# Kernel tuning notes

Measured on AMD Instinct MI355X. Metric: run time of the kernel, lower is better.

## Reference

```python
import jax, jax.numpy as jnp
import numpy as np

# module constants (from init_kwargs)
CS, NV, ED = 8, 4, 32          # codebook_size, num_variables, embedding_dim
VIEWS, D, KSZ = 3, 16, 3        # num_input_channels, depth, kernel_size
HW = 14                         # 7 * scale (scale=2)
CSP = 8                         # spatial of conv_shape after three valid 3x3 convs: 14->12->10->8
KSTATES = CS ** NV              # 4096 combinatorial discrete states


def _elu(x):
    return jnp.where(x > 0, x, jnp.expm1(x))


def _conv_t(x, w, b):
    # PyTorch ConvTranspose2d(stride=1, padding=0); w: (Cin, Cout, k, k)
    wf = jnp.flip(w, (2, 3)).transpose(1, 0, 2, 3)  # -> (Cout, Cin, k, k)
    p = w.shape[2] - 1
    y = jax.lax.conv_general_dilated(x, wf, (1, 1), [(p, p), (p, p)],
                                     dimension_numbers=('NCHW', 'OIHW', 'NCHW'))
    return y + b[None, :, None, None]


def setup_inputs() -> dict:
    key = jax.random.key(0)
    ks = jax.random.split(key, 10)
    rn = lambda k, shape, s=1.0: jax.random.normal(k, shape, jnp.float32) * s
    return {
        'x': rn(ks[0], (64, VIEWS, HW, HW)),
        'latent_embedding': rn(ks[1], (NV, CS, ED)),
        'lin_w': rn(ks[2], (VIEWS, ED * NV, 4 * D * CSP * CSP), 0.05),
        'lin_b': rn(ks[3], (VIEWS, 4 * D * CSP * CSP), 0.05),
        'w1': rn(ks[4], (VIEWS, 4 * D, 2 * D, KSZ, KSZ), 0.05),
        'b1': rn(ks[5], (VIEWS, 2 * D), 0.05),
        'w2': rn(ks[6], (VIEWS, 2 * D, D, KSZ, KSZ), 0.05),
        'b2': rn(ks[7], (VIEWS, D), 0.05),
        'w3': rn(ks[8], (VIEWS, D, 1, KSZ, KSZ), 0.05),
        'b3': rn(ks[9], (VIEWS, 1), 0.05),
    }


def reference(x, latent_embedding, lin_w, lin_b, w1, b1, w2, b2, w3, b3):
    # all combinations of codebook indices (itertools.product order): [K, NV]
    all_idcs = jnp.stack(
        jnp.meshgrid(*([jnp.arange(CS)] * NV), indexing='ij'), -1).reshape(-1, NV)
    # gather: z[k, v, :] = latent_embedding[v, all_idcs[k, v], :]
    z = latent_embedding[jnp.arange(NV)[None, :], all_idcs]       # [K, NV, ED]
    zf = z.reshape(KSTATES, NV * ED)                              # 'b n d -> b (n d)'

    def decode(lw, lb, W1, B1, W2, B2, W3, B3):
        h = (zf @ lw + lb).reshape(KSTATES, 4 * D, CSP, CSP)
        h = _elu(_conv_t(h, W1, B1))
        h = _elu(_conv_t(h, W2, B2))
        h = _conv_t(h, W3, B3)
        return h[:, 0]                                            # [K, HW, HW]

    m = jax.vmap(decode)(lin_w, lin_b, w1, b1, w2, b2, w3, b3)    # [views, K, HW, HW]
    m = jnp.transpose(m, (1, 0, 2, 3))                            # [K, views, HW, HW]

    # obs_logits = -0.5 * sum_{h,w} (m[None] - x[:, None])**2, computed without
    # materializing the [B, K, views, HW, HW] broadcast tensor
    m2 = jnp.sum(m * m, axis=(-2, -1))                            # [K, views]
    x2 = jnp.sum(x * x, axis=(-2, -1))                            # [B, views]
    cross = jnp.einsum('kvhw,bvhw->bkv', m, x)                    # [B, K, views]
    return -0.5 * (m2[None] + x2[:, None] - 2.0 * cross)          # [B, K, views]
```

## Files before the change

### kernel.cpp

```cpp
#include <hip/hip_runtime.h>
#include <cstddef>


typedef __attribute__((ext_vector_type(4))) float f32x4;
typedef _Float16 half8v __attribute__((ext_vector_type(8)));
typedef _Float16 half4v __attribute__((ext_vector_type(4)));
typedef _Float16 half2v __attribute__((ext_vector_type(2)));

static __device__ __forceinline__ float elu(float s) {
    float e = __expf(s) - 1.0f;
    return s > 0.f ? s : e;
}
static __device__ __forceinline__ float dot2acc(int hpair, int wpair, float acc) {
#if __has_builtin(__builtin_amdgcn_fdot2)
    return __builtin_amdgcn_fdot2(__builtin_bit_cast(half2v, hpair),
                                  __builtin_bit_cast(half2v, wpair), acc, false);
#else
    half2v h = __builtin_bit_cast(half2v, hpair);
    half2v w = __builtin_bit_cast(half2v, wpair);
    acc = fmaf((float)h.x, (float)w.x, acc);
    return fmaf((float)h.y, (float)w.y, acc);
#endif
}

__global__ __launch_bounds__(256) void pre_kernel(const float* __restrict__ x,
                                                  float* __restrict__ x2,
                                                  short* __restrict__ xB,
                                                  const float* __restrict__ w2,
                                                  short* __restrict__ Wf) {
    int v = blockIdx.x;
    int part = blockIdx.y;
    int t = threadIdx.x;
    if (part < 4) {
        int nb = part;
        short* xBv = xB + v * 14336 + nb * 3584;
        for (int idx = t; idx < 3584; idx += 256) {
            int j = idx & 7, lane = (idx >> 3) & 63, s = idx >> 9;
            int px = s * 32 + ((lane >> 4) << 3) + j;
            int b  = nb * 16 + (lane & 15);
            float val = (px < 196) ? x[(b * 3 + v) * 196 + px] : 0.f;
            _Float16 h = (_Float16)val;
            xBv[idx] = __builtin_bit_cast(short, h);
        }
    } else if (part == 4) {
        int w = t >> 6, lane = t & 63;
        for (int b = w; b < 64; b += 4) {
            const float* xp = x + (b * 3 + v) * 196;
            float s = 0.f;
            for (int px = lane; px < 196; px += 64) s = fmaf(xp[px], xp[px], s);
#pragma unroll
            for (int off = 32; off; off >>= 1) s += __shfl_down(s, off, 64);
            if (lane == 0) x2[v * 64 + b] = s;
        }
    } else if (t < 64) {
        int lane = t;
        const float* w2v = w2 + v * 32 * 16 * 9;
        int co = lane & 15;
        int cibase = (lane >> 4) * 8;
#pragma unroll
        for (int tap = 0; tap < 9; ++tap)
#pragma unroll
            for (int j = 0; j < 8; ++j) {
                _Float16 h = (_Float16)w2v[((cibase + j) * 16 + co) * 9 + tap];
                Wf[(((v * 9 + tap) * 64 + lane) << 3) + j] = __builtin_bit_cast(short, h);
            }
    }
}

__global__ __launch_bounds__(256) void pmat_kernel(const float* __restrict__ le,
                                                   const float* __restrict__ lin_w,
                                                   float* __restrict__ P3) {
    int o  = blockIdx.x * 256 + threadIdx.x;
    int vc = blockIdx.y;
    int v  = blockIdx.z;
    int vp = vc >> 3;
    const float* lwv = lin_w + (size_t)v * 128 * 4096;
    const float* lep = le + vc * 32;
    float acc = 0.f;
#pragma unroll
    for (int e = 0; e < 32; ++e)
        acc = fmaf(lep[e], lwv[(vp * 32 + e) * 4096 + o], acc);
    P3[((size_t)v * 32 + vc) * 4096 + o] = acc;
}

__global__ __launch_bounds__(320) void fold1_kernel(const float* __restrict__ P3,
                                                    const float* __restrict__ lin_b,
                                                    const float* __restrict__ w1,
                                                    const float* __restrict__ b1,
                                                    float* __restrict__ Qa,
                                                    float* __restrict__ Qb) {
    __shared__ float sPt[64 * 144];
    __shared__ float sW[16 * 32 * 9];
    int row = blockIdx.x;
    int v   = blockIdx.y;
    int z   = blockIdx.z;
    int t = threadIdx.x;
    const float* src = (row < 32) ? (P3 + ((size_t)v * 32 + row) * 4096)
                                  : (lin_b + v * 4096);
    float4* zp = (float4*)sPt;
    for (int i = t; i < 2304; i += 320) zp[i] = float4{0.f, 0.f, 0.f, 0.f};
    __syncthreads();
    for (int i = t; i < 4096; i += 320) {
        int ci = i >> 6, r = i & 63, y = r >> 3, xx = r & 7;
        sPt[ci * 144 + (xx + 2) * 12 + (y + 2)] = src[i];
    }
    const float* w1v = w1 + (size_t)v * 64 * 32 * 9;
    int co = t / 10, ox = t % 10;
    float acc[10];
#pragma unroll
    for (int i = 0; i < 10; ++i) acc[i] = 0.f;

    for (int c0 = z * 2; c0 < z * 2 + 2; ++c0) {
        __syncthreads();
        for (int i = t; i < 4608; i += 320) sW[i] = w1v[c0 * 4608 + i];
        __syncthreads();
#pragma unroll 2
        for (int ci = 0; ci < 16; ++ci) {
            const float* xp = sPt + (c0 * 16 + ci) * 144;
            const float* wp = sW + (ci * 32 + co) * 9;
            float wv[9];
#pragma unroll
            for (int j = 0; j < 9; ++j) wv[j] = wp[j];
#pragma unroll
            for (int b = 0; b < 3; ++b) {
                const float* colp = xp + (ox + 2 - b) * 12;
                float4 c0v = *(const float4*)(colp);
                float4 c1v = *(const float4*)(colp + 4);
                float4 c2v = *(const float4*)(colp + 8);
                float cv[12] = {c0v.x, c0v.y, c0v.z, c0v.w,
                                c1v.x, c1v.y, c1v.z, c1v.w,
                                c2v.x, c2v.y, c2v.z, c2v.w};
#pragma unroll
                for (int a = 0; a < 3; ++a) {
                    float wgt = wv[a * 3 + b];
#pragma unroll
                    for (int oy = 0; oy < 10; ++oy)
                        acc[oy] = fmaf(cv[oy + 2 - a], wgt, acc[oy]);
                }
            }
        }
    }
    float bb = (z == 0 && row == 32) ? b1[v * 32 + co] : 0.f;
    float* dst = (z == 0 ? Qa : Qb) + (size_t)v * 105600 + row * 3200;
#pragma unroll
    for (int oy = 0; oy < 10; ++oy)
        dst[(ox * 10 + oy) * 32 + co] = acc[oy] + bb;
}

__global__ __launch_bounds__(256) void pair_kernel(const float* __restrict__ Qa,
                                                   const float* __restrict__ Qb,
                                                   float* __restrict__ Q01,
                                                   float* __restrict__ Q23b) {
    int p = blockIdx.x;
    int half = blockIdx.y;
    int v = blockIdx.z;
    const float4* basea = (const float4*)(Qa + (size_t)v * 105600);
    const float4* baseb = (const float4*)(Qb + (size_t)v * 105600);
    if (half == 0) {
        const float4* ra = basea + (p >> 3) * 800;
        const float4* rb = baseb + (p >> 3) * 800;
        const float4* rc = basea + (8 + (p & 7)) * 800;
        const float4* rd = baseb + (8 + (p & 7)) * 800;
        float4* dst = (float4*)(Q01 + (size_t)v * 204800 + p * 3200);
        for (int i = threadIdx.x; i < 800; i += 256) {
            float4 a = ra[i], b = rb[i], c = rc[i], d = rd[i];
            dst[i] = float4{a.x + b.x + c.x + d.x, a.y + b.y + c.y + d.y,
                            a.z + b.z + c.z + d.z, a.w + b.w + c.w + d.w};
        }
    } else {
        const float4* ra = basea + (16 + (p >> 3)) * 800;
        const float4* rb = baseb + (16 + (p >> 3)) * 800;
        const float4* rc = basea + (24 + (p & 7)) * 800;
        const float4* rd = baseb + (24 + (p & 7)) * 800;
        const float4* re = basea + 32 * 800;
        const float4* rf = baseb + 32 * 800;
        float4* dst = (float4*)(Q23b + (size_t)v * 204800 + p * 3200);
        for (int i = threadIdx.x; i < 800; i += 256) {
            float4 a = ra[i], b = rb[i], c = rc[i], d = rd[i], e = re[i], f = rf[i];
            dst[i] = float4{a.x + b.x + c.x + d.x + e.x + f.x,
                            a.y + b.y + c.y + d.y + e.y + f.y,
                            a.z + b.z + c.z + d.z + e.z + f.z,
                            a.w + b.w + c.w + d.w + e.w + f.w};
        }
    }
}

__global__ __launch_bounds__(256) void fused_kernel(const float* __restrict__ Q01,
                                                    const float* __restrict__ Q23b,
                                                    const short* __restrict__ Wf,
                                                    const float* __restrict__ b2,
                                                    const float* __restrict__ w3,
                                                    const float* __restrict__ b3,
                                                    short* __restrict__ Mh,
                                                    float* __restrict__ m2g) {
    __shared__ alignas(16) short sH1[196 * 40];
    __shared__ alignas(16) short sH2[16 * 392];
    __shared__ int sW3p[72];
    __shared__ float sM2;
    int k = blockIdx.x;
    int v = blockIdx.y;
    int t = threadIdx.x;
    int lane = t & 63;
    int g = lane >> 4;

    half8v bfrag[9];
#pragma unroll
    for (int tap = 0; tap < 9; ++tap)
        bfrag[tap] = *(const half8v*)(const void*)(Wf + (((v * 9 + tap) * 64 + lane) << 3));
    float bias2 = b2[v * 16 + (lane & 15)];

    if (t == 0) sM2 = 0.f;
    for (int pix = t; pix < 196; pix += 256) {
        int c = pix / 14, r = pix % 14;
        if (c < 2 || c >= 12 || r < 2 || r >= 12) {
            int4* z = (int4*)(sH1 + pix * 40);
            z[0] = int4{0,0,0,0}; z[1] = int4{0,0,0,0};
            z[2] = int4{0,0,0,0}; z[3] = int4{0,0,0,0};
        }
    }
    {
        int pix = t;
        int c = pix >> 4, r = pix & 15;
        if (c < 2 || c >= 14 || r < 2 || r >= 14) {
            int4* z = (int4*)(sH2 + c * 392 + r * 24);
            z[0] = int4{0,0,0,0}; z[1] = int4{0,0,0,0};
        }
    }
    if (t < 72) {
        int tap = t / 8, j = t % 8;
        half2v p = {(_Float16)w3[v * 144 + (2 * j) * 9 + tap],
                    (_Float16)w3[v * 144 + (2 * j + 1) * 9 + tap]};
        sW3p[t] = __builtin_bit_cast(int, p);
    }

    {
        const float4* qa = (const float4*)(Q01  + ((size_t)v * 64 + (k >> 6)) * 3200);
        const float4* qb = (const float4*)(Q23b + ((size_t)v * 64 + (k & 63)) * 3200);
        int ci4 = (t & 7) * 4;
        int pix = t >> 3;
        int cx = pix / 10, ry = pix % 10;
        for (int i = t; i < 800; i += 256) {
            float4 a = qa[i], b = qb[i];
            half4v o = {(_Float16)elu(a.x + b.x), (_Float16)elu(a.y + b.y),
                        (_Float16)elu(a.z + b.z), (_Float16)elu(a.w + b.w)};
            *(half4v*)(void*)(sH1 + ((cx + 2) * 14 + (ry + 2)) * 40 + ci4) = o;
            cx += 3; ry += 2;
            if (ry >= 10) { ry -= 10; ++cx; }
        }
    }
    __syncthreads();

    {
        int w = t >> 6;
        for (int tile = w; tile < 9; tile += 4) {
            int m = tile * 16 + (lane & 15);
            int cx2 = m / 12, ry2 = m % 12;
            const short* basemin = sH1 + (cx2 * 14 + ry2) * 40 + g * 8;
            f32x4 acc0 = {bias2, bias2, bias2, bias2};
            f32x4 acc1 = {0.f, 0.f, 0.f, 0.f};
#pragma unroll
            for (int a = 0; a < 3; ++a)
#pragma unroll
                for (int b = 0; b < 3; ++b) {
                    half8v af = *(const half8v*)(const void*)(basemin + ((2 - b) * 14 + (2 - a)) * 40);
                    int idx = a * 3 + b;
                    if (idx & 1)
                        acc1 = __builtin_amdgcn_mfma_f32_16x16x32_f16(af, bfrag[idx], acc1, 0, 0, 0);
                    else
                        acc0 = __builtin_amdgcn_mfma_f32_16x16x32_f16(af, bfrag[idx], acc0, 0, 0, 0);
                }
            int p0 = tile * 16 + g * 4;
            int cxp = p0 / 12, ryp = p0 % 12;
            int co = lane & 15;
#pragma unroll
            for (int r = 0; r < 4; ++r) {
                _Float16 h = (_Float16)elu(acc0[r] + acc1[r]);
                sH2[(cxp + 2) * 392 + (ryp + 2) * 24 + co] = __builtin_bit_cast(short, h);
                ++ryp; if (ryp == 12) { ryp = 0; ++cxp; }
            }
        }
    }
    __syncthreads();

    {
        float mval = 0.f;
        if (t < 196) {
            float bias3 = b3[v];
            int ry3 = t / 14, cx3 = t % 14;
            float a0 = bias3, a1 = 0.f, a2 = 0.f, a3 = 0.f;
#pragma unroll
            for (int a = 0; a < 3; ++a)
#pragma unroll
                for (int b = 0; b < 3; ++b) {
                    const short* base = sH2 + (cx3 + 2 - b) * 392 + (ry3 + 2 - a) * 24;
                    int4 lo = *(const int4*)(const void*)(base);
                    int4 hi = *(const int4*)(const void*)(base + 8);
                    const int* wp = sW3p + (a * 3 + b) * 8;
                    a0 = dot2acc(lo.x, wp[0], a0);
                    a1 = dot2acc(lo.y, wp[1], a1);
                    a2 = dot2acc(lo.z, wp[2], a2);
                    a3 = dot2acc(lo.w, wp[3], a3);
                    a0 = dot2acc(hi.x, wp[4], a0);
                    a1 = dot2acc(hi.y, wp[5], a1);
                    a2 = dot2acc(hi.z, wp[6], a2);
                    a3 = dot2acc(hi.w, wp[7], a3);
                }
            mval = (a0 + a1) + (a2 + a3);
        }
        if (t < 224) {
            _Float16 h = (_Float16)mval;
            Mh[((size_t)v * 4096 + k) * 224 + t] = __builtin_bit_cast(short, h);
        }
        float sq = mval * mval;
#pragma unroll
        for (int off = 32; off; off >>= 1) sq += __shfl_down(sq, off, 64);
        if (lane == 0) atomicAdd(&sM2, sq);
        __syncthreads();
        if (t == 0) m2g[(size_t)v * 4096 + k] = sM2;
    }
}

__global__ __launch_bounds__(256) void gemm_final_kernel(const short* __restrict__ Mh,
                                                         const short* __restrict__ xB,
                                                         const float* __restrict__ m2g,
                                                         const float* __restrict__ x2g,
                                                         float* __restrict__ out) {
    __shared__ float sC[3 * 64 * 17];
    __shared__ float sM2t[48];
    int t = threadIdx.x, lane = t & 63, nb = t >> 6;
    int k0 = blockIdx.x * 16;
    if (t < 48) {
        int v = t % 3, kk = t / 3;
        sM2t[kk * 3 + v] = m2g[(size_t)v * 4096 + k0 + kk];
    }
    int mrow = lane & 15;
    int g = lane >> 4;
#pragma unroll
    for (int v = 0; v < 3; ++v) {
        f32x4 acc = {0.f, 0.f, 0.f, 0.f};
        const short* abase = Mh + ((size_t)v * 4096 + k0 + mrow) * 224 + g * 8;
        const short* bbase = xB + (((v * 4 + nb) * 7) * 64 + lane) * 8;
#pragma unroll
        for (int s = 0; s < 7; ++s) {
            half8v af = *(const half8v*)(const void*)(abase + s * 32);
            half8v bf = *(const half8v*)(const void*)(bbase + s * 512);
            acc = __builtin_amdgcn_mfma_f32_16x16x32_f16(af, bf, acc, 0, 0, 0);
        }
        int b = nb * 16 + mrow;
#pragma unroll
        for (int r = 0; r < 4; ++r)
            sC[(v * 64 + b) * 17 + g * 4 + r] = acc[r];
    }
    __syncthreads();
    int b = t >> 2, q = t & 3;
    float x2v0 = x2g[b], x2v1 = x2g[64 + b], x2v2 = x2g[128 + b];
    float buf[12];
#pragma unroll
    for (int i = 0; i < 4; ++i) {
        int kk = q * 4 + i;
        buf[i * 3 + 0] = sC[(0 * 64 + b) * 17 + kk] - 0.5f * (sM2t[kk * 3 + 0] + x2v0);
        buf[i * 3 + 1] = sC[(1 * 64 + b) * 17 + kk] - 0.5f * (sM2t[kk * 3 + 1] + x2v1);
        buf[i * 3 + 2] = sC[(2 * 64 + b) * 17 + kk] - 0.5f * (sM2t[kk * 3 + 2] + x2v2);
    }
    float* dst = out + ((size_t)b * 4096 + k0) * 3 + q * 12;
    *(float4*)(dst)     = float4{buf[0], buf[1], buf[2],  buf[3]};
    *(float4*)(dst + 4) = float4{buf[4], buf[5], buf[6],  buf[7]};
    *(float4*)(dst + 8) = float4{buf[8], buf[9], buf[10], buf[11]};
}

extern "C" void kernel_launch(void* const* d_in, const int* in_sizes, int n_in,
                              void* d_out, int out_size, void* d_ws, size_t ws_size,
                              hipStream_t stream) {
    const float* x     = (const float*)d_in[0];
    const float* le    = (const float*)d_in[1];
    const float* lin_w = (const float*)d_in[2];
    const float* lin_b = (const float*)d_in[3];
    const float* w1    = (const float*)d_in[4];
    const float* b1    = (const float*)d_in[5];
    const float* w2    = (const float*)d_in[6];
    const float* b2    = (const float*)d_in[7];
    const float* w3    = (const float*)d_in[8];
    const float* b3    = (const float*)d_in[9];
    float* out = (float*)d_out;

    float* ws = (float*)d_ws;
    float* x2g  = ws;
    short* xB   = (short*)(ws + 192);
    short* Wf   = (short*)(ws + 21760);
    float* P3   = ws + 28736;
    float* Qa   = ws + 421952;
    float* Qb   = ws + 738752;
    float* Q01  = ws + 1055552;
    float* Q23b = ws + 1669952;
    short* Mh   = (short*)(ws + 2284352);
    float* m2g  = ws + 3660608;

    pre_kernel<<<dim3(3, 6), 256, 0, stream>>>(x, x2g, xB, w2, Wf);
    pmat_kernel<<<dim3(16, 32, 3), 256, 0, stream>>>(le, lin_w, P3);
    fold1_kernel<<<dim3(33, 3, 2), 320, 0, stream>>>(P3, lin_b, w1, b1, Qa, Qb);
    pair_kernel<<<dim3(64, 2, 3), 256, 0, stream>>>(Qa, Qb, Q01, Q23b);
    fused_kernel<<<dim3(4096, 3), 256, 0, stream>>>(Q01, Q23b, Wf, b2, w3, b3, Mh, m2g);
    gemm_final_kernel<<<256, 256, 0, stream>>>(Mh, xB, m2g, x2g, out);
}
```

Baseline: 199.7 us.

## Fuse pre, pmat and fold1 kernels into one prep kernel; swizzle sH2 layout

The x/weight preprocessing, the latent-embedding×lin_w projection and the first transposed-conv fold are merged into a single 216-block launch. The projection is computed in registers and written straight into shared memory, so the P3 buffer and two kernel launches go away. The fold blocks each recompute their projection row (duplicated across the two z halves), which adds redundant lin_w reads. Separately, the sH2 shared-memory layout in the fused kernel gets an XOR-like row offset, meant to reduce bank conflicts in the ELU store and the conv3 reads.

```diff
diff --git a/kernel.cpp b/kernel.cpp
--- a/kernel.cpp
+++ b/kernel.cpp
@@ -22,87 +22,100 @@
     return fmaf((float)h.y, (float)w.y, acc);
 #endif
 }
-
-__global__ __launch_bounds__(256) void pre_kernel(const float* __restrict__ x,
-                                                  float* __restrict__ x2,
-                                                  short* __restrict__ xB,
-                                                  const float* __restrict__ w2,
-                                                  short* __restrict__ Wf) {
-    int v = blockIdx.x;
-    int part = blockIdx.y;
+static __device__ __forceinline__ int sh2addr(int c, int r) {
+    return c * 392 + r * 24 + (((r >> 2) & 3) << 3);
+}
+
+__global__ __launch_bounds__(320) void prep_kernel(const float* __restrict__ x,
+                                                   const float* __restrict__ le,
+                                                   const float* __restrict__ lin_w,
+                                                   const float* __restrict__ lin_b,
+                                                   const float* __restrict__ w1,
+                                                   const float* __restrict__ b1,
+                                                   const float* __restrict__ w2,
+                                                   float* __restrict__ Qa,
+                                                   float* __restrict__ Qb,
+                                                   float* __restrict__ x2,
+                                                   short* __restrict__ xB,
+                                                   short* __restrict__ Wf) {
+    int bid = blockIdx.x;
     int t = threadIdx.x;
-    if (part < 4) {
-        int nb = part;
-        short* xBv = xB + v * 14336 + nb * 3584;
-        for (int idx = t; idx < 3584; idx += 256) {
-            int j = idx & 7, lane = (idx >> 3) & 63, s = idx >> 9;
-            int px = s * 32 + ((lane >> 4) << 3) + j;
-            int b  = nb * 16 + (lane & 15);
-            float val = (px < 196) ? x[(b * 3 + v) * 196 + px] : 0.f;
-            _Float16 h = (_Float16)val;
-            xBv[idx] = __builtin_bit_cast(short, h);
-        }
-    } else if (part == 4) {
-        int w = t >> 6, lane = t & 63;
-        for (int b = w; b < 64; b += 4) {
-            const float* xp = x + (b * 3 + v) * 196;
-            float s = 0.f;
-            for (int px = lane; px < 196; px += 64) s = fmaf(xp[px], xp[px], s);
-#pragma unroll
-            for (int off = 32; off; off >>= 1) s += __shfl_down(s, off, 64);
-            if (lane == 0) x2[v * 64 + b] = s;
-        }
-    } else if (t < 64) {
-        int lane = t;
-        const float* w2v = w2 + v * 32 * 16 * 9;
-        int co = lane & 15;
-        int cibase = (lane >> 4) * 8;
-#pragma unroll
-        for (int tap = 0; tap < 9; ++tap)
-#pragma unroll
-            for (int j = 0; j < 8; ++j) {
-                _Float16 h = (_Float16)w2v[((cibase + j) * 16 + co) * 9 + tap];
-                Wf[(((v * 9 + tap) * 64 + lane) << 3) + j] = __builtin_bit_cast(short, h);
+    if (bid >= 198) {
+        int pid = bid - 198;
+        int v = pid % 3, part = pid / 3;
+        if (part < 4) {
+            int nb = part;
+            short* xBv = xB + v * 14336 + nb * 3584;
+            for (int idx = t; idx < 3584; idx += 320) {
+                int j = idx & 7, lane = (idx >> 3) & 63, s = idx >> 9;
+                int px = s * 32 + ((lane >> 4) << 3) + j;
+                int b  = nb * 16 + (lane & 15);
+                float val = (px < 196) ? x[(b * 3 + v) * 196 + px] : 0.f;
+                _Float16 h = (_Float16)val;
+                xBv[idx] = __builtin_bit_cast(short, h);
             }
-    }
-}
-
-__global__ __launch_bounds__(256) void pmat_kernel(const float* __restrict__ le,
-                                                   const float* __restrict__ lin_w,
-                                                   float* __restrict__ P3) {
-    int o  = blockIdx.x * 256 + threadIdx.x;
-    int vc = blockIdx.y;
-    int v  = blockIdx.z;
-    int vp = vc >> 3;
-    const float* lwv = lin_w + (size_t)v * 128 * 4096;
-    const float* lep = le + vc * 32;
-    float acc = 0.f;
-#pragma unroll
-    for (int e = 0; e < 32; ++e)
-        acc = fmaf(lep[e], lwv[(vp * 32 + e) * 4096 + o], acc);
-    P3[((size_t)v * 32 + vc) * 4096 + o] = acc;
-}
-
-__global__ __launch_bounds__(320) void fold1_kernel(const float* __restrict__ P3,
-                                                    const float* __restrict__ lin_b,
-                                                    const float* __restrict__ w1,
-                                                    const float* __restrict__ b1,
-                                                    float* __restrict__ Qa,
-                                                    float* __restrict__ Qb) {
+        } else if (part == 4) {
+            int w = t >> 6, lane = t & 63;
+            for (int b = w; b < 64; b += 5) {
+                const float* xp = x + (b * 3 + v) * 196;
+                float s = 0.f;
+                for (int px = lane; px < 196; px += 64) s = fmaf(xp[px], xp[px], s);
+#pragma unroll
+                for (int off = 32; off; off >>= 1) s += __shfl_down(s, off, 64);
+                if (lane == 0) x2[v * 64 + b] = s;
+            }
+        } else if (t < 64) {
+            int lane = t;
+            const float* w2v = w2 + v * 32 * 16 * 9;
+            int co = lane & 15;
+            int cibase = (lane >> 4) * 8;
+#pragma unroll
+            for (int tap = 0; tap < 9; ++tap)
+#pragma unroll
+                for (int j = 0; j < 8; ++j) {
+                    _Float16 h = (_Float16)w2v[((cibase + j) * 16 + co) * 9 + tap];
+                    Wf[(((v * 9 + tap) * 64 + lane) << 3) + j] = __builtin_bit_cast(short, h);
+                }
+        }
+        return;
+    }
     __shared__ float sPt[64 * 144];
     __shared__ float sW[16 * 32 * 9];
-    int row = blockIdx.x;
-    int v   = blockIdx.y;
-    int z   = blockIdx.z;
-    int t = threadIdx.x;
-    const float* src = (row < 32) ? (P3 + ((size_t)v * 32 + row) * 4096)
-                                  : (lin_b + v * 4096);
+    int row = bid % 33;
+    int v   = (bid / 33) % 3;
+    int z   = bid / 99;
+
+    float pacc[16];
+    if (t < 256) {
+        if (row < 32) {
+            int vp = row >> 3;
+            const float* base0 = lin_w + (size_t)v * 524288 + (size_t)vp * 32 * 4096 + t;
+            const float* lep = le + row * 32;
+#pragma unroll
+            for (int j = 0; j < 16; ++j) pacc[j] = 0.f;
+            for (int e = 0; e < 32; ++e) {
+                float lv = lep[e];
+                const float* bp = base0 + e * 4096;
+#pragma unroll
+                for (int j = 0; j < 16; ++j)
+                    pacc[j] = fmaf(lv, bp[j * 256], pacc[j]);
+            }
+        } else {
+            const float* bp = lin_b + v * 4096 + t;
+#pragma unroll
+            for (int j = 0; j < 16; ++j) pacc[j] = bp[j * 256];
+        }
+    }
     float4* zp = (float4*)sPt;
     for (int i = t; i < 2304; i += 320) zp[i] = float4{0.f, 0.f, 0.f, 0.f};
     __syncthreads();
-    for (int i = t; i < 4096; i += 320) {
-        int ci = i >> 6, r = i & 63, y = r >> 3, xx = r & 7;
-        sPt[ci * 144 + (xx + 2) * 12 + (y + 2)] = src[i];
+    if (t < 256) {
+#pragma unroll
+        for (int j = 0; j < 16; ++j) {
+            int i = t + j * 256;
+            int ci = i >> 6, r = i & 63, y = r >> 3, xx = r & 7;
+            sPt[ci * 144 + (xx + 2) * 12 + (y + 2)] = pacc[j];
+        }
     }
     const float* w1v = w1 + (size_t)v * 64 * 32 * 9;
     int co = t / 10, ox = t % 10;
@@ -194,7 +207,7 @@
                                                     short* __restrict__ Mh,
                                                     float* __restrict__ m2g) {
     __shared__ alignas(16) short sH1[196 * 40];
-    __shared__ alignas(16) short sH2[16 * 392];
+    __shared__ alignas(16) short sH2[6280];
     __shared__ int sW3p[72];
     __shared__ float sM2;
     int k = blockIdx.x;
@@ -222,7 +235,7 @@
         int pix = t;
         int c = pix >> 4, r = pix & 15;
         if (c < 2 || c >= 14 || r < 2 || r >= 14) {
-            int4* z = (int4*)(sH2 + c * 392 + r * 24);
+            int4* z = (int4*)(sH2 + sh2addr(c, r));
             z[0] = int4{0,0,0,0}; z[1] = int4{0,0,0,0};
         }
     }
@@ -275,7 +288,7 @@
 #pragma unroll
             for (int r = 0; r < 4; ++r) {
                 _Float16 h = (_Float16)elu(acc0[r] + acc1[r]);
-                sH2[(cxp + 2) * 392 + (ryp + 2) * 24 + co] = __builtin_bit_cast(short, h);
+                sH2[sh2addr(cxp + 2, ryp + 2) + co] = __builtin_bit_cast(short, h);
                 ++ryp; if (ryp == 12) { ryp = 0; ++cxp; }
             }
         }
@@ -292,7 +305,7 @@
             for (int a = 0; a < 3; ++a)
 #pragma unroll
                 for (int b = 0; b < 3; ++b) {
-                    const short* base = sH2 + (cx3 + 2 - b) * 392 + (ry3 + 2 - a) * 24;
+                    const short* base = sH2 + sh2addr(cx3 + 2 - b, ry3 + 2 - a);
                     int4 lo = *(const int4*)(const void*)(base);
                     int4 hi = *(const int4*)(const void*)(base + 8);
                     const int* wp = sW3p + (a * 3 + b) * 8;
@@ -387,17 +400,15 @@
     float* x2g  = ws;
     short* xB   = (short*)(ws + 192);
     short* Wf   = (short*)(ws + 21760);
-    float* P3   = ws + 28736;
-    float* Qa   = ws + 421952;
-    float* Qb   = ws + 738752;
-    float* Q01  = ws + 1055552;
-    float* Q23b = ws + 1669952;
-    short* Mh   = (short*)(ws + 2284352);
-    float* m2g  = ws + 3660608;
-
-    pre_kernel<<<dim3(3, 6), 256, 0, stream>>>(x, x2g, xB, w2, Wf);
-    pmat_kernel<<<dim3(16, 32, 3), 256, 0, stream>>>(le, lin_w, P3);
-    fold1_kernel<<<dim3(33, 3, 2), 320, 0, stream>>>(P3, lin_b, w1, b1, Qa, Qb);
+    float* Qa   = ws + 28736;
+    float* Qb   = ws + 345536;
+    float* Q01  = ws + 662336;
+    float* Q23b = ws + 1276736;
+    short* Mh   = (short*)(ws + 1891136);
+    float* m2g  = ws + 3267392;
+
+    prep_kernel<<<216, 320, 0, stream>>>(x, le, lin_w, lin_b, w1, b1, w2,
+                                         Qa, Qb, x2g, xB, Wf);
     pair_kernel<<<dim3(64, 2, 3), 256, 0, stream>>>(Qa, Qb, Q01, Q23b);
     fused_kernel<<<dim3(4096, 3), 256, 0, stream>>>(Q01, Q23b, Wf, b2, w3, b3, Mh, m2g);
     gemm_final_kernel<<<256, 256, 0, stream>>>(Mh, xB, m2g, x2g, out);
```

Result: faster. 180.6 us (-9.6%).
